# Kernel optimization log

Measured on AMD Instinct MI355X. Metric: run time of the kernel, lower is better.

The kernel has to match this reference:

```python
import jax, jax.numpy as jnp
import numpy as np

B, K, E = 32768, 100, 64
N_USERS, N_ITEMS = 100000, 50000
MLP_DIMS = [2, 20, 200, 200, 20, 1]  # input_dim=2 -> x10 -> x100 -> x100 -> x10 -> output_dim=1


def setup_inputs() -> dict:
    key = jax.random.key(0)
    ks = jax.random.split(key, 20)
    inp = {
        "user_idxs": jax.random.randint(ks[0], (B,), 0, N_USERS),
        "item_idxs": jax.random.randint(ks[1], (B,), 0, N_ITEMS),
        "user_idx_tensor": jax.random.randint(ks[2], (N_USERS, K), 0, N_USERS),
        "item_idx_tensor": jax.random.randint(ks[3], (N_ITEMS, K), 0, N_ITEMS),
        # nn.Embedding default init: N(0, 1)
        "user_emb": jax.random.normal(ks[4], (N_USERS, E), dtype=jnp.float32),
        "item_emb": jax.random.normal(ks[5], (N_ITEMS, E), dtype=jnp.float32),
    }
    # nn.Linear default init: U(-1/sqrt(fan_in), 1/sqrt(fan_in))
    for i in range(5):
        fan_in, fan_out = MLP_DIMS[i], MLP_DIMS[i + 1]
        bound = 1.0 / np.sqrt(fan_in)
        inp[f"w{i+1}"] = jax.random.uniform(ks[6 + i], (fan_out, fan_in), minval=-bound, maxval=bound, dtype=jnp.float32)
        inp[f"b{i+1}"] = jax.random.uniform(ks[11 + i], (fan_out,), minval=-bound, maxval=bound, dtype=jnp.float32)
    return inp


def _concat_mlp(x, w1, b1, w2, b2, w3, b3, w4, b4, w5, b5):
    # x: [B, E, 2] -> [B, E, 1]
    h = jax.nn.relu(x @ w1.T + b1)
    h = jax.nn.relu(h @ w2.T + b2)
    h = jax.nn.relu(h @ w3.T + b3)
    h = jax.nn.relu(h @ w4.T + b4)
    return h @ w5.T + b5


def reference(user_idxs, item_idxs, user_idx_tensor, item_idx_tensor,
              user_emb, item_emb,
              w1, b1, w2, b2, w3, b3, w4, b4, w5, b5):
    user_neighs = user_idx_tensor[user_idxs]          # [B, K]
    user_sum = user_emb[user_neighs].sum(axis=1)      # [B, E]
    item_neighs = item_idx_tensor[item_idxs]          # [B, K]
    item_sum = item_emb[item_neighs].sum(axis=1)      # [B, E]
    # cat along dim 1 with keepdim then permute(0,2,1) == stack along last axis
    x = jnp.stack([user_sum, item_sum], axis=-1)      # [B, E, 2]
    concat = _concat_mlp(x, w1, b1, w2, b2, w3, b3, w4, b4, w5, b5)  # [B, E, 1]
    return jax.nn.sigmoid(concat.mean(axis=1)).squeeze(-1)           # [B]
```

## Files before the change

kernel.cpp:

```cpp
#include <hip/hip_runtime.h>
#include <hip/hip_bf16.h>
#include <math.h>

typedef short v8s __attribute__((ext_vector_type(8)));
typedef float v4f __attribute__((ext_vector_type(4)));
typedef unsigned int v4u __attribute__((ext_vector_type(4)));
typedef unsigned short us;
typedef unsigned int uu;

#define MFMA16(a,b,c) __builtin_amdgcn_mfma_f32_16x16x32_bf16((a),(b),(c),0,0,0)

#define W3F_ELEMS (7*13*512)
#define W2F_ELEMS (13*512)
#define W4F_ELEMS (14*512)
#define WALL_ELEMS (W3F_ELEMS + W2F_ELEMS + W4F_ELEMS)
#define OFF_W3F 0
#define OFF_W2F (OFF_W3F + W3F_ELEMS*2)
#define OFF_W4F (OFF_W2F + W2F_ELEMS*2)
#define OFF_B2B (OFF_W4F + W4F_ELEMS*2)
#define OFF_B3B (OFF_B2B + 208*4)
#define OFF_B4B (OFF_B3B + 224*4)
#define OFF_W5B (OFF_B4B + 32*4)
#define OFF_W1P (OFF_W5B + 32*4)
#define OFF_X   (256*1024)
#define CB_ELEMS 592
#define CB_B3 208
#define CB_B4 432
#define CB_W5 464
#define CB_W1 496

__device__ __forceinline__ us f2bf(float f) {
    union { float f; unsigned int u; } v; v.f = f;
    unsigned int u = v.u + 0x7FFFu + ((v.u >> 16) & 1u);
    return (us)(u >> 16);
}
__device__ __forceinline__ uu pack2bf(float a, float b) {
    union { __hip_bfloat162 v; uu u; } cv;
    cv.v.x = __float2bfloat16(a);
    cv.v.y = __float2bfloat16(b);
    return cv.u;
}
__device__ __forceinline__ us f2h(float f) {
    _Float16 h = (_Float16)f;
    return *(us*)&h;
}

__global__ void prep_conv_kernel(
    const float* __restrict__ w1, const float* __restrict__ b1,
    const float* __restrict__ w2, const float* __restrict__ w3,
    const float* __restrict__ w4, const float* __restrict__ b2,
    const float* __restrict__ b3, const float* __restrict__ b4,
    const float* __restrict__ w5, char* __restrict__ ws,
    const float* __restrict__ uemb, const float* __restrict__ iemb,
    _Float16* __restrict__ ue16, _Float16* __restrict__ ie16,
    int nu64, int ni64)
{
    us* w3f = (us*)(ws + OFF_W3F);
    us* w2f = (us*)(ws + OFF_W2F);
    us* w4f = (us*)(ws + OFF_W4F);
    float* b2b = (float*)(ws + OFF_B2B);
    float* b3b = (float*)(ws + OFF_B3B);
    float* b4b = (float*)(ws + OFF_B4B);
    float* w5b = (float*)(ws + OFF_W5B);
    float* w1p = (float*)(ws + OFF_W1P);

    const int gid = blockIdx.x * blockDim.x + threadIdx.x;
    const int stride = gridDim.x * blockDim.x;

    for (int i = gid*4; i < nu64; i += stride*4) {
        float4 v = *(const float4*)(uemb + i);
        ushort4 o = { f2h(v.x), f2h(v.y), f2h(v.z), f2h(v.w) };
        *(ushort4*)((us*)ue16 + i) = o;
    }
    for (int i = gid*4; i < ni64; i += stride*4) {
        float4 v = *(const float4*)(iemb + i);
        ushort4 o = { f2h(v.x), f2h(v.y), f2h(v.z), f2h(v.w) };
        *(ushort4*)((us*)ie16 + i) = o;
    }

    for (int idx = gid; idx < W3F_ELEMS; idx += stride) {
        int i = idx & 7, lane = (idx >> 3) & 63, f = idx >> 9;
        int nt3 = f % 13, t = f / 13;
        int cc = lane & 15, gg = lane >> 4;
        int j = 16*nt3 + cc;
        int k = 32*t + 16*(i >> 2) + 4*gg + (i & 3);
        w3f[idx] = f2bf((j < 200 && k < 200) ? w3[j*200 + k] : 0.f);
    }
    for (int idx = gid; idx < W2F_ELEMS; idx += stride) {
        int i = idx & 7, lane = (idx >> 3) & 63, nt = idx >> 9;
        int j = 16*nt + (lane & 15), k = 8*(lane >> 4) + i;
        w2f[idx] = f2bf((j < 200 && k < 20) ? w2[j*20 + k] : 0.f);
    }
    for (int idx = gid; idx < W4F_ELEMS; idx += stride) {
        int i = idx & 7, lane = (idx >> 3) & 63, f = idx >> 9;
        int t = f >> 1, jt = f & 1;
        int cc = lane & 15, gg = lane >> 4;
        int j = 16*jt + cc;
        int k = 32*t + 16*(i >> 2) + 4*gg + (i & 3);
        w4f[idx] = f2bf((j < 20 && k < 200) ? w4[j*200 + k] : 0.f);
    }
    for (int i = gid; i < 208; i += stride) b2b[i] = (i < 200) ? b2[i] : 0.f;
    for (int i = gid; i < 224; i += stride) b3b[i] = (i < 200) ? b3[i] : 0.f;
    for (int i = gid; i < 32;  i += stride) b4b[i] = (i < 20) ? b4[i] : 0.f;
    for (int i = gid; i < 32;  i += stride) w5b[i] = (i < 20) ? w5[i] : 0.f;
    for (int i = gid; i < 96;  i += stride) {
        int q = i >> 5, r = i & 31;
        float v = 0.f;
        if (r < 20) v = (q == 0) ? w1[2*r] : (q == 1) ? w1[2*r + 1] : b1[r];
        w1p[i] = v;
    }
}

__global__ __launch_bounds__(256, 8) void gather_kernel(
    const int* __restrict__ user_idxs, const int* __restrict__ item_idxs,
    const int* __restrict__ uidx, const int* __restrict__ iidx,
    const _Float16* __restrict__ ue16, const _Float16* __restrict__ ie16,
    float* __restrict__ xu, float* __restrict__ xi, int B)
{
    const int tid  = (int)threadIdx.x;
    const int lane = tid & 63;
    const int task = (int)blockIdx.x * 4 + (tid >> 6);
    if (task >= 2*B) return;
    const int b = task >> 1;
    const bool isItem = task & 1;

    const int* nrow = isItem ? (iidx + (size_t)item_idxs[b]*100)
                             : (uidx + (size_t)user_idxs[b]*100);
    const _Float16* emb = isItem ? ie16 : ue16;

    float a0=0.f,a1=0.f,a2=0.f,a3=0.f,a4=0.f,a5=0.f,a6=0.f,a7=0.f;
    #pragma unroll 2
    for (int k = 0; k < 96; k += 16) {
        int4 i0 = *(const int4*)(nrow + k);
        int4 i1 = *(const int4*)(nrow + k + 4);
        int4 i2 = *(const int4*)(nrow + k + 8);
        int4 i3 = *(const int4*)(nrow + k + 12);
        a0 += (float)emb[(size_t)i0.x*64 + lane];
        a1 += (float)emb[(size_t)i0.y*64 + lane];
        a2 += (float)emb[(size_t)i0.z*64 + lane];
        a3 += (float)emb[(size_t)i0.w*64 + lane];
        a4 += (float)emb[(size_t)i1.x*64 + lane];
        a5 += (float)emb[(size_t)i1.y*64 + lane];
        a6 += (float)emb[(size_t)i1.z*64 + lane];
        a7 += (float)emb[(size_t)i1.w*64 + lane];
        a0 += (float)emb[(size_t)i2.x*64 + lane];
        a1 += (float)emb[(size_t)i2.y*64 + lane];
        a2 += (float)emb[(size_t)i2.z*64 + lane];
        a3 += (float)emb[(size_t)i2.w*64 + lane];
        a4 += (float)emb[(size_t)i3.x*64 + lane];
        a5 += (float)emb[(size_t)i3.y*64 + lane];
        a6 += (float)emb[(size_t)i3.z*64 + lane];
        a7 += (float)emb[(size_t)i3.w*64 + lane];
    }
    int4 it = *(const int4*)(nrow + 96);
    a0 += (float)emb[(size_t)it.x*64 + lane];
    a1 += (float)emb[(size_t)it.y*64 + lane];
    a2 += (float)emb[(size_t)it.z*64 + lane];
    a3 += (float)emb[(size_t)it.w*64 + lane];

    float s = ((a0+a4)+(a1+a5)) + ((a2+a6)+(a3+a7));
    (isItem ? xi : xu)[(size_t)b*64 + lane] = s;
}

__device__ __forceinline__ void make_b1f4(float su, float si, int c, int g,
                                          const float* __restrict__ w1p,
                                          v4u b1f[4])
{
    const v4f wx0 = *(const v4f*)(w1p + 8*g);
    const v4f wx1 = *(const v4f*)(w1p + 8*g + 4);
    const v4f wy0 = *(const v4f*)(w1p + 32 + 8*g);
    const v4f wy1 = *(const v4f*)(w1p + 32 + 8*g + 4);
    const v4f wb0 = *(const v4f*)(w1p + 64 + 8*g);
    const v4f wb1 = *(const v4f*)(w1p + 64 + 8*g + 4);
    #pragma unroll
    for (int m = 0; m < 4; ++m) {
        const float xu = __shfl(su, 16*m + c);
        const float xv = __shfl(si, 16*m + c);
        float h0 = fmaxf(fmaf(xu, wx0[0], fmaf(xv, wy0[0], wb0[0])), 0.f);
        float h1 = fmaxf(fmaf(xu, wx0[1], fmaf(xv, wy0[1], wb0[1])), 0.f);
        float h2 = fmaxf(fmaf(xu, wx0[2], fmaf(xv, wy0[2], wb0[2])), 0.f);
        float h3 = fmaxf(fmaf(xu, wx0[3], fmaf(xv, wy0[3], wb0[3])), 0.f);
        float h4 = fmaxf(fmaf(xu, wx1[0], fmaf(xv, wy1[0], wb1[0])), 0.f);
        float h5 = fmaxf(fmaf(xu, wx1[1], fmaf(xv, wy1[1], wb1[1])), 0.f);
        float h6 = fmaxf(fmaf(xu, wx1[2], fmaf(xv, wy1[2], wb1[2])), 0.f);
        float h7 = fmaxf(fmaf(xu, wx1[3], fmaf(xv, wy1[3], wb1[3])), 0.f);
        b1f[m] = (v4u){ pack2bf(h0,h1), pack2bf(h2,h3),
                        pack2bf(h4,h5), pack2bf(h6,h7) };
    }
}

__global__ __launch_bounds__(512, 2) void mlp_kernel(
    const float* __restrict__ xu, const float* __restrict__ xi,
    const float* __restrict__ b5p, const char* __restrict__ ws,
    float* __restrict__ out, int B, int NIT)
{
    __shared__ us wall[WALL_ELEMS];
    __shared__ __align__(16) float cbuf[CB_ELEMS];

    const int tid  = (int)threadIdx.x;
    const int lane = tid & 63;
    const int wv   = __builtin_amdgcn_readfirstlane(tid >> 6);
    const int c = lane & 15;
    const int g = lane >> 4;
    const int wstep = (int)gridDim.x * 8;

    {
        const us* src = (const us*)(ws + OFF_W3F);
        for (int s = tid; s < WALL_ELEMS/8; s += 512)
            *(v8s*)(wall + s*8) = *(const v8s*)(src + s*8);
        const float* csrc = (const float*)(ws + OFF_B2B);
        for (int s = tid; s < CB_ELEMS; s += 512)
            cbuf[s] = csrc[s];
    }
    const us* w3l = wall;
    const us* w2l = wall + W3F_ELEMS;
    const us* w4l = wall + W3F_ELEMS + W2F_ELEMS;
    const float b5v = b5p[0];

    int b = (int)blockIdx.x*8 + wv;
    int bc = (b < B) ? b : (B - 1);
    float su = xu[(size_t)bc*64 + lane];
    float si = xi[(size_t)bc*64 + lane];
    __syncthreads();

    #pragma unroll 1
    for (int it = 0; it < NIT; ++it) {
        const int nb = b + wstep;
        const int nbc = (nb < B) ? nb : (B - 1);
        const bool more = (it + 1 < NIT);

        v4u b1f[4];
        make_b1f4(su, si, c, g, cbuf + CB_W1, b1f);

        v4u b2f[4][7];
        __builtin_amdgcn_s_setprio(1);
        #pragma unroll
        for (int t = 0; t < 6; ++t) {
            v8s afa = *(const v8s*)(w2l + ((2*t)*64   + lane)*8);
            v8s afb = *(const v8s*)(w2l + ((2*t+1)*64 + lane)*8);
            v4f bva = *(const v4f*)(cbuf + 32*t + 4*g);
            v4f bvb = *(const v4f*)(cbuf + 32*t + 16 + 4*g);
            #pragma unroll
            for (int m = 0; m < 4; ++m) {
                v8s bb = __builtin_bit_cast(v8s, b1f[m]);
                v4f aa = MFMA16(afa, bb, bva);
                v4f ab = MFMA16(afb, bb, bvb);
                b2f[m][t] = (v4u){ pack2bf(fmaxf(aa[0],0.f), fmaxf(aa[1],0.f)),
                                   pack2bf(fmaxf(aa[2],0.f), fmaxf(aa[3],0.f)),
                                   pack2bf(fmaxf(ab[0],0.f), fmaxf(ab[1],0.f)),
                                   pack2bf(fmaxf(ab[2],0.f), fmaxf(ab[3],0.f)) };
            }
        }
        {
            v8s afa = *(const v8s*)(w2l + (12*64 + lane)*8);
            v4f bva = *(const v4f*)(cbuf + 192 + 4*g);
            #pragma unroll
            for (int m = 0; m < 4; ++m) {
                v8s bb = __builtin_bit_cast(v8s, b1f[m]);
                v4f aa = MFMA16(afa, bb, bva);
                b2f[m][6] = (v4u){ pack2bf(fmaxf(aa[0],0.f), fmaxf(aa[1],0.f)),
                                   pack2bf(fmaxf(aa[2],0.f), fmaxf(aa[3],0.f)),
                                   0u, 0u };
            }
        }
        __builtin_amdgcn_s_setprio(0);

        float nsu = 0.f, nsi = 0.f;
        if (more) {
            nsu = xu[(size_t)nbc*64 + lane];
            nsi = xi[(size_t)nbc*64 + lane];
        }

        v4f acc4[4][2];
        v4f bc0 = *(const v4f*)(cbuf + CB_B4 + 4*g);
        v4f bc1 = *(const v4f*)(cbuf + CB_B4 + 16 + 4*g);
        #pragma unroll
        for (int p = 0; p < 7; ++p) {
            v8s a40 = *(const v8s*)(w4l + ((2*p)*64   + lane)*8);
            v8s a41 = *(const v8s*)(w4l + ((2*p+1)*64 + lane)*8);

            v4f acc3[4][2];
            __builtin_amdgcn_s_setprio(1);
            {
                v8s af0 = *(const v8s*)(w3l + ((2*p)*64 + lane)*8);
                v4f bv0 = *(const v4f*)(cbuf + CB_B3 + 16*(2*p) + 4*g);
                #pragma unroll
                for (int m = 0; m < 4; ++m)
                    acc3[m][0] = MFMA16(af0, __builtin_bit_cast(v8s, b2f[m][0]), bv0);
                if (p < 6) {
                    v8s af1 = *(const v8s*)(w3l + ((2*p+1)*64 + lane)*8);
                    v4f bv1 = *(const v4f*)(cbuf + CB_B3 + 16*(2*p+1) + 4*g);
                    #pragma unroll
                    for (int m = 0; m < 4; ++m)
                        acc3[m][1] = MFMA16(af1, __builtin_bit_cast(v8s, b2f[m][0]), bv1);
                }
            }
            #pragma unroll
            for (int ksc = 1; ksc < 7; ++ksc) {
                v8s af0 = *(const v8s*)(w3l + ((ksc*13 + 2*p)*64 + lane)*8);
                #pragma unroll
                for (int m = 0; m < 4; ++m)
                    acc3[m][0] = MFMA16(af0, __builtin_bit_cast(v8s, b2f[m][ksc]), acc3[m][0]);
                if (p < 6) {
                    v8s af1 = *(const v8s*)(w3l + ((ksc*13 + 2*p+1)*64 + lane)*8);
                    #pragma unroll
                    for (int m = 0; m < 4; ++m)
                        acc3[m][1] = MFMA16(af1, __builtin_bit_cast(v8s, b2f[m][ksc]), acc3[m][1]);
                }
            }
            __builtin_amdgcn_s_setprio(0);
            #pragma unroll
            for (int m = 0; m < 4; ++m) {
                v4u bfu;
                if (p < 6) {
                    bfu = (v4u){
                        pack2bf(fmaxf(acc3[m][0][0],0.f), fmaxf(acc3[m][0][1],0.f)),
                        pack2bf(fmaxf(acc3[m][0][2],0.f), fmaxf(acc3[m][0][3],0.f)),
                        pack2bf(fmaxf(acc3[m][1][0],0.f), fmaxf(acc3[m][1][1],0.f)),
                        pack2bf(fmaxf(acc3[m][1][2],0.f), fmaxf(acc3[m][1][3],0.f)) };
                } else {
                    bfu = (v4u){
                        pack2bf(fmaxf(acc3[m][0][0],0.f), fmaxf(acc3[m][0][1],0.f)),
                        pack2bf(fmaxf(acc3[m][0][2],0.f), fmaxf(acc3[m][0][3],0.f)),
                        0u, 0u };
                }
                v8s bb = __builtin_bit_cast(v8s, bfu);
                acc4[m][0] = MFMA16(a40, bb, (p == 0) ? bc0 : acc4[m][0]);
                acc4[m][1] = MFMA16(a41, bb, (p == 0) ? bc1 : acc4[m][1]);
            }
        }

        __builtin_amdgcn_sched_barrier(0);

        v4f w5lo = *(const v4f*)(cbuf + CB_W5 + 4*g);
        v4f w5hi = *(const v4f*)(cbuf + CB_W5 + 16 + 4*g);
        float s = 0.f;
        #pragma unroll
        for (int m = 0; m < 4; ++m) {
            #pragma unroll
            for (int q = 0; q < 4; ++q) {
                float h0 = fmaxf(acc4[m][0][q], 0.f);
                float h1 = fmaxf(acc4[m][1][q], 0.f);
                s = fmaf(h0, w5lo[q], fmaf(h1, w5hi[q], s));
            }
        }
        #pragma unroll
        for (int off = 1; off < 64; off <<= 1) s += __shfl_xor(s, off);
        if (lane == 0 && b < B)
            out[b] = 1.0f / (1.0f + expf(-(s * (1.0f / 64.0f) + b5v)));

        su = nsu; si = nsi; b = nb;
    }
}

extern "C" void kernel_launch(void* const* d_in, const int* in_sizes, int n_in,
                              void* d_out, int out_size, void* d_ws, size_t ws_size,
                              hipStream_t stream) {
    const int*   user_idxs = (const int*)d_in[0];
    const int*   item_idxs = (const int*)d_in[1];
    const int*   uidx      = (const int*)d_in[2];
    const int*   iidx      = (const int*)d_in[3];
    const float* uemb      = (const float*)d_in[4];
    const float* iemb      = (const float*)d_in[5];
    const float* w1 = (const float*)d_in[6];
    const float* b1 = (const float*)d_in[7];
    const float* w2 = (const float*)d_in[8];
    const float* b2 = (const float*)d_in[9];
    const float* w3 = (const float*)d_in[10];
    const float* b3 = (const float*)d_in[11];
    const float* w4 = (const float*)d_in[12];
    const float* b4 = (const float*)d_in[13];
    const float* w5 = (const float*)d_in[14];
    const float* b5 = (const float*)d_in[15];
    float* out = (float*)d_out;
    char* ws = (char*)d_ws;

    const int B    = in_sizes[0];
    const int nu64 = in_sizes[4];
    const int ni64 = in_sizes[5];

    float* xu = (float*)(ws + OFF_X);
    float* xi = xu + (size_t)B * 64;
    _Float16* ue16 = (_Float16*)(ws + OFF_X + (size_t)2 * B * 64 * 4);
    _Float16* ie16 = ue16 + nu64;

    hipLaunchKernelGGL(prep_conv_kernel, dim3(1024), dim3(256), 0, stream,
                       w1, b1, w2, w3, w4, b2, b3, b4, w5, ws,
                       uemb, iemb, ue16, ie16, nu64, ni64);

    const int ntask = 2 * B;
    hipLaunchKernelGGL(gather_kernel, dim3((ntask + 3) / 4), dim3(256), 0, stream,
                       user_idxs, item_idxs, uidx, iidx, ue16, ie16, xu, xi, B);

    const int GRID = 256;
    const int rows_per_iter = GRID * 8;
    const int NIT = (B + rows_per_iter - 1) / rows_per_iter;
    hipLaunchKernelGGL(mlp_kernel, dim3(GRID), dim3(512), 0, stream,
                       xu, xi, b5, ws, out, B, NIT);
}
```

Baseline: 326.6 us.

## Split per-row MLP into two half passes to cut registers and raise waves per block

The MLP body now handles each batch row's 64 embedding dims in two passes of 32 instead of one pass of 64, which halves the live b2f/acc3/acc4 register arrays. This register saving is used to raise the block size from 512 to 768 threads (12 waves, 12 rows per block per iteration) with launch bounds (768,3). The aim is more resident waves to hide MFMA and LDS latency. In exchange each pass reloads the weight fragments from LDS twice per row, and the next-row prefetch is now issued between the two passes.

```diff
diff --git a/kernel.cpp b/kernel.cpp
--- a/kernel.cpp
+++ b/kernel.cpp
@@ -162,9 +162,10 @@
     (isItem ? xi : xu)[(size_t)b*64 + lane] = s;
 }
 
-__device__ __forceinline__ void make_b1f4(float su, float si, int c, int g,
+template <int P>
+__device__ __forceinline__ void make_b1f2(float su, float si, int c, int g,
                                           const float* __restrict__ w1p,
-                                          v4u b1f[4])
+                                          v4u b1f[2])
 {
     const v4f wx0 = *(const v4f*)(w1p + 8*g);
     const v4f wx1 = *(const v4f*)(w1p + 8*g + 4);
@@ -173,9 +174,9 @@
     const v4f wb0 = *(const v4f*)(w1p + 64 + 8*g);
     const v4f wb1 = *(const v4f*)(w1p + 64 + 8*g + 4);
     #pragma unroll
-    for (int m = 0; m < 4; ++m) {
-        const float xu = __shfl(su, 16*m + c);
-        const float xv = __shfl(si, 16*m + c);
+    for (int m = 0; m < 2; ++m) {
+        const float xu = __shfl(su, 32*P + 16*m + c);
+        const float xv = __shfl(si, 32*P + 16*m + c);
         float h0 = fmaxf(fmaf(xu, wx0[0], fmaf(xv, wy0[0], wb0[0])), 0.f);
         float h1 = fmaxf(fmaf(xu, wx0[1], fmaf(xv, wy0[1], wb0[1])), 0.f);
         float h2 = fmaxf(fmaf(xu, wx0[2], fmaf(xv, wy0[2], wb0[2])), 0.f);
@@ -189,7 +190,119 @@
     }
 }
 
-__global__ __launch_bounds__(512, 2) void mlp_kernel(
+__device__ __forceinline__ float mlp_pass2(
+    const v4u b1f[2],
+    const us* __restrict__ w3l, const us* __restrict__ w2l,
+    const us* __restrict__ w4l, const float* __restrict__ cbuf,
+    const int lane, const int g)
+{
+    const v8s bb0 = __builtin_bit_cast(v8s, b1f[0]);
+    const v8s bb1 = __builtin_bit_cast(v8s, b1f[1]);
+
+    v4u b2f[2][7];
+    __builtin_amdgcn_s_setprio(1);
+    #pragma unroll
+    for (int t = 0; t < 6; ++t) {
+        v8s afa = *(const v8s*)(w2l + ((2*t)*64   + lane)*8);
+        v8s afb = *(const v8s*)(w2l + ((2*t+1)*64 + lane)*8);
+        v4f bva = *(const v4f*)(cbuf + 32*t + 4*g);
+        v4f bvb = *(const v4f*)(cbuf + 32*t + 16 + 4*g);
+        v4f aa0 = MFMA16(afa, bb0, bva);
+        v4f aa1 = MFMA16(afa, bb1, bva);
+        v4f ab0 = MFMA16(afb, bb0, bvb);
+        v4f ab1 = MFMA16(afb, bb1, bvb);
+        b2f[0][t] = (v4u){ pack2bf(fmaxf(aa0[0],0.f), fmaxf(aa0[1],0.f)),
+                           pack2bf(fmaxf(aa0[2],0.f), fmaxf(aa0[3],0.f)),
+                           pack2bf(fmaxf(ab0[0],0.f), fmaxf(ab0[1],0.f)),
+                           pack2bf(fmaxf(ab0[2],0.f), fmaxf(ab0[3],0.f)) };
+        b2f[1][t] = (v4u){ pack2bf(fmaxf(aa1[0],0.f), fmaxf(aa1[1],0.f)),
+                           pack2bf(fmaxf(aa1[2],0.f), fmaxf(aa1[3],0.f)),
+                           pack2bf(fmaxf(ab1[0],0.f), fmaxf(ab1[1],0.f)),
+                           pack2bf(fmaxf(ab1[2],0.f), fmaxf(ab1[3],0.f)) };
+    }
+    {
+        v8s afa = *(const v8s*)(w2l + (12*64 + lane)*8);
+        v4f bva = *(const v4f*)(cbuf + 192 + 4*g);
+        v4f aa0 = MFMA16(afa, bb0, bva);
+        v4f aa1 = MFMA16(afa, bb1, bva);
+        b2f[0][6] = (v4u){ pack2bf(fmaxf(aa0[0],0.f), fmaxf(aa0[1],0.f)),
+                           pack2bf(fmaxf(aa0[2],0.f), fmaxf(aa0[3],0.f)), 0u, 0u };
+        b2f[1][6] = (v4u){ pack2bf(fmaxf(aa1[0],0.f), fmaxf(aa1[1],0.f)),
+                           pack2bf(fmaxf(aa1[2],0.f), fmaxf(aa1[3],0.f)), 0u, 0u };
+    }
+    __builtin_amdgcn_s_setprio(0);
+
+    v4f acc4[2][2];
+    v4f bc0 = *(const v4f*)(cbuf + CB_B4 + 4*g);
+    v4f bc1 = *(const v4f*)(cbuf + CB_B4 + 16 + 4*g);
+    #pragma unroll
+    for (int p = 0; p < 7; ++p) {
+        v8s a40 = *(const v8s*)(w4l + ((2*p)*64   + lane)*8);
+        v8s a41 = *(const v8s*)(w4l + ((2*p+1)*64 + lane)*8);
+
+        v4f acc3[2][2];
+        __builtin_amdgcn_s_setprio(1);
+        {
+            v8s af0 = *(const v8s*)(w3l + ((2*p)*64 + lane)*8);
+            v4f bv0 = *(const v4f*)(cbuf + CB_B3 + 16*(2*p) + 4*g);
+            acc3[0][0] = MFMA16(af0, __builtin_bit_cast(v8s, b2f[0][0]), bv0);
+            acc3[1][0] = MFMA16(af0, __builtin_bit_cast(v8s, b2f[1][0]), bv0);
+            if (p < 6) {
+                v8s af1 = *(const v8s*)(w3l + ((2*p+1)*64 + lane)*8);
+                v4f bv1 = *(const v4f*)(cbuf + CB_B3 + 16*(2*p+1) + 4*g);
+                acc3[0][1] = MFMA16(af1, __builtin_bit_cast(v8s, b2f[0][0]), bv1);
+                acc3[1][1] = MFMA16(af1, __builtin_bit_cast(v8s, b2f[1][0]), bv1);
+            }
+        }
+        #pragma unroll
+        for (int ksc = 1; ksc < 7; ++ksc) {
+            v8s af0 = *(const v8s*)(w3l + ((ksc*13 + 2*p)*64 + lane)*8);
+            acc3[0][0] = MFMA16(af0, __builtin_bit_cast(v8s, b2f[0][ksc]), acc3[0][0]);
+            acc3[1][0] = MFMA16(af0, __builtin_bit_cast(v8s, b2f[1][ksc]), acc3[1][0]);
+            if (p < 6) {
+                v8s af1 = *(const v8s*)(w3l + ((ksc*13 + 2*p+1)*64 + lane)*8);
+                acc3[0][1] = MFMA16(af1, __builtin_bit_cast(v8s, b2f[0][ksc]), acc3[0][1]);
+                acc3[1][1] = MFMA16(af1, __builtin_bit_cast(v8s, b2f[1][ksc]), acc3[1][1]);
+            }
+        }
+        __builtin_amdgcn_s_setprio(0);
+        #pragma unroll
+        for (int m = 0; m < 2; ++m) {
+            v4u bfu;
+            if (p < 6) {
+                bfu = (v4u){
+                    pack2bf(fmaxf(acc3[m][0][0],0.f), fmaxf(acc3[m][0][1],0.f)),
+                    pack2bf(fmaxf(acc3[m][0][2],0.f), fmaxf(acc3[m][0][3],0.f)),
+                    pack2bf(fmaxf(acc3[m][1][0],0.f), fmaxf(acc3[m][1][1],0.f)),
+                    pack2bf(fmaxf(acc3[m][1][2],0.f), fmaxf(acc3[m][1][3],0.f)) };
+            } else {
+                bfu = (v4u){
+                    pack2bf(fmaxf(acc3[m][0][0],0.f), fmaxf(acc3[m][0][1],0.f)),
+                    pack2bf(fmaxf(acc3[m][0][2],0.f), fmaxf(acc3[m][0][3],0.f)),
+                    0u, 0u };
+            }
+            v8s bb = __builtin_bit_cast(v8s, bfu);
+            acc4[m][0] = MFMA16(a40, bb, (p == 0) ? bc0 : acc4[m][0]);
+            acc4[m][1] = MFMA16(a41, bb, (p == 0) ? bc1 : acc4[m][1]);
+        }
+    }
+
+    v4f w5lo = *(const v4f*)(cbuf + CB_W5 + 4*g);
+    v4f w5hi = *(const v4f*)(cbuf + CB_W5 + 16 + 4*g);
+    float s = 0.f;
+    #pragma unroll
+    for (int m = 0; m < 2; ++m) {
+        #pragma unroll
+        for (int q = 0; q < 4; ++q) {
+            float h0 = fmaxf(acc4[m][0][q], 0.f);
+            float h1 = fmaxf(acc4[m][1][q], 0.f);
+            s = fmaf(h0, w5lo[q], fmaf(h1, w5hi[q], s));
+        }
+    }
+    return s;
+}
+
+__global__ __launch_bounds__(768, 3) void mlp_kernel(
     const float* __restrict__ xu, const float* __restrict__ xi,
     const float* __restrict__ b5p, const char* __restrict__ ws,
     float* __restrict__ out, int B, int NIT)
@@ -202,14 +315,14 @@
     const int wv   = __builtin_amdgcn_readfirstlane(tid >> 6);
     const int c = lane & 15;
     const int g = lane >> 4;
-    const int wstep = (int)gridDim.x * 8;
+    const int wstep = (int)gridDim.x * 12;
 
     {
         const us* src = (const us*)(ws + OFF_W3F);
-        for (int s = tid; s < WALL_ELEMS/8; s += 512)
+        for (int s = tid; s < WALL_ELEMS/8; s += 768)
             *(v8s*)(wall + s*8) = *(const v8s*)(src + s*8);
         const float* csrc = (const float*)(ws + OFF_B2B);
-        for (int s = tid; s < CB_ELEMS; s += 512)
+        for (int s = tid; s < CB_ELEMS; s += 768)
             cbuf[s] = csrc[s];
     }
     const us* w3l = wall;
@@ -217,7 +330,7 @@
     const us* w4l = wall + W3F_ELEMS + W2F_ELEMS;
     const float b5v = b5p[0];
 
-    int b = (int)blockIdx.x*8 + wv;
+    int b = (int)blockIdx.x*12 + wv;
     int bc = (b < B) ? b : (B - 1);
     float su = xu[(size_t)bc*64 + lane];
     float si = xi[(size_t)bc*64 + lane];
@@ -229,121 +342,22 @@
         const int nbc = (nb < B) ? nb : (B - 1);
         const bool more = (it + 1 < NIT);
 
-        v4u b1f[4];
-        make_b1f4(su, si, c, g, cbuf + CB_W1, b1f);
-
-        v4u b2f[4][7];
-        __builtin_amdgcn_s_setprio(1);
-        #pragma unroll
-        for (int t = 0; t < 6; ++t) {
-            v8s afa = *(const v8s*)(w2l + ((2*t)*64   + lane)*8);
-            v8s afb = *(const v8s*)(w2l + ((2*t+1)*64 + lane)*8);
-            v4f bva = *(const v4f*)(cbuf + 32*t + 4*g);
-            v4f bvb = *(const v4f*)(cbuf + 32*t + 16 + 4*g);
-            #pragma unroll
-            for (int m = 0; m < 4; ++m) {
-                v8s bb = __builtin_bit_cast(v8s, b1f[m]);
-                v4f aa = MFMA16(afa, bb, bva);
-                v4f ab = MFMA16(afb, bb, bvb);
-                b2f[m][t] = (v4u){ pack2bf(fmaxf(aa[0],0.f), fmaxf(aa[1],0.f)),
-                                   pack2bf(fmaxf(aa[2],0.f), fmaxf(aa[3],0.f)),
-                                   pack2bf(fmaxf(ab[0],0.f), fmaxf(ab[1],0.f)),
-                                   pack2bf(fmaxf(ab[2],0.f), fmaxf(ab[3],0.f)) };
-            }
-        }
-        {
-            v8s afa = *(const v8s*)(w2l + (12*64 + lane)*8);
-            v4f bva = *(const v4f*)(cbuf + 192 + 4*g);
-            #pragma unroll
-            for (int m = 0; m < 4; ++m) {
-                v8s bb = __builtin_bit_cast(v8s, b1f[m]);
-                v4f aa = MFMA16(afa, bb, bva);
-                b2f[m][6] = (v4u){ pack2bf(fmaxf(aa[0],0.f), fmaxf(aa[1],0.f)),
-                                   pack2bf(fmaxf(aa[2],0.f), fmaxf(aa[3],0.f)),
-                                   0u, 0u };
-            }
-        }
-        __builtin_amdgcn_s_setprio(0);
+        v4u b1f[2];
+        make_b1f2<0>(su, si, c, g, cbuf + CB_W1, b1f);
+        float s = mlp_pass2(b1f, w3l, w2l, w4l, cbuf, lane, g);
+
+        __builtin_amdgcn_sched_barrier(0);
 
         float nsu = 0.f, nsi = 0.f;
         if (more) {
             nsu = xu[(size_t)nbc*64 + lane];
             nsi = xi[(size_t)nbc*64 + lane];
         }
-
-        v4f acc4[4][2];
-        v4f bc0 = *(const v4f*)(cbuf + CB_B4 + 4*g);
-        v4f bc1 = *(const v4f*)(cbuf + CB_B4 + 16 + 4*g);
-        #pragma unroll
-        for (int p = 0; p < 7; ++p) {
-            v8s a40 = *(const v8s*)(w4l + ((2*p)*64   + lane)*8);
-            v8s a41 = *(const v8s*)(w4l + ((2*p+1)*64 + lane)*8);
-
-            v4f acc3[4][2];
-            __builtin_amdgcn_s_setprio(1);
-            {
-                v8s af0 = *(const v8s*)(w3l + ((2*p)*64 + lane)*8);
-                v4f bv0 = *(const v4f*)(cbuf + CB_B3 + 16*(2*p) + 4*g);
-                #pragma unroll
-                for (int m = 0; m < 4; ++m)
-                    acc3[m][0] = MFMA16(af0, __builtin_bit_cast(v8s, b2f[m][0]), bv0);
-                if (p < 6) {
-                    v8s af1 = *(const v8s*)(w3l + ((2*p+1)*64 + lane)*8);
-                    v4f bv1 = *(const v4f*)(cbuf + CB_B3 + 16*(2*p+1) + 4*g);
-                    #pragma unroll
-                    for (int m = 0; m < 4; ++m)
-                        acc3[m][1] = MFMA16(af1, __builtin_bit_cast(v8s, b2f[m][0]), bv1);
-                }
-            }
-            #pragma unroll
-            for (int ksc = 1; ksc < 7; ++ksc) {
-                v8s af0 = *(const v8s*)(w3l + ((ksc*13 + 2*p)*64 + lane)*8);
-                #pragma unroll
-                for (int m = 0; m < 4; ++m)
-                    acc3[m][0] = MFMA16(af0, __builtin_bit_cast(v8s, b2f[m][ksc]), acc3[m][0]);
-                if (p < 6) {
-                    v8s af1 = *(const v8s*)(w3l + ((ksc*13 + 2*p+1)*64 + lane)*8);
-                    #pragma unroll
-                    for (int m = 0; m < 4; ++m)
-                        acc3[m][1] = MFMA16(af1, __builtin_bit_cast(v8s, b2f[m][ksc]), acc3[m][1]);
-                }
-            }
-            __builtin_amdgcn_s_setprio(0);
-            #pragma unroll
-            for (int m = 0; m < 4; ++m) {
-                v4u bfu;
-                if (p < 6) {
-                    bfu = (v4u){
-                        pack2bf(fmaxf(acc3[m][0][0],0.f), fmaxf(acc3[m][0][1],0.f)),
-                        pack2bf(fmaxf(acc3[m][0][2],0.f), fmaxf(acc3[m][0][3],0.f)),
-                        pack2bf(fmaxf(acc3[m][1][0],0.f), fmaxf(acc3[m][1][1],0.f)),
-                        pack2bf(fmaxf(acc3[m][1][2],0.f), fmaxf(acc3[m][1][3],0.f)) };
-                } else {
-                    bfu = (v4u){
-                        pack2bf(fmaxf(acc3[m][0][0],0.f), fmaxf(acc3[m][0][1],0.f)),
-                        pack2bf(fmaxf(acc3[m][0][2],0.f), fmaxf(acc3[m][0][3],0.f)),
-                        0u, 0u };
-                }
-                v8s bb = __builtin_bit_cast(v8s, bfu);
-                acc4[m][0] = MFMA16(a40, bb, (p == 0) ? bc0 : acc4[m][0]);
-                acc4[m][1] = MFMA16(a41, bb, (p == 0) ? bc1 : acc4[m][1]);
-            }
-        }
+        make_b1f2<1>(su, si, c, g, cbuf + CB_W1, b1f);
+        s += mlp_pass2(b1f, w3l, w2l, w4l, cbuf, lane, g);
 
         __builtin_amdgcn_sched_barrier(0);
 
-        v4f w5lo = *(const v4f*)(cbuf + CB_W5 + 4*g);
-        v4f w5hi = *(const v4f*)(cbuf + CB_W5 + 16 + 4*g);
-        float s = 0.f;
-        #pragma unroll
-        for (int m = 0; m < 4; ++m) {
-            #pragma unroll
-            for (int q = 0; q < 4; ++q) {
-                float h0 = fmaxf(acc4[m][0][q], 0.f);
-                float h1 = fmaxf(acc4[m][1][q], 0.f);
-                s = fmaf(h0, w5lo[q], fmaf(h1, w5hi[q], s));
-            }
-        }
         #pragma unroll
         for (int off = 1; off < 64; off <<= 1) s += __shfl_xor(s, off);
         if (lane == 0 && b < B)
@@ -393,8 +407,8 @@
                        user_idxs, item_idxs, uidx, iidx, ue16, ie16, xu, xi, B);
 
     const int GRID = 256;
-    const int rows_per_iter = GRID * 8;
+    const int rows_per_iter = GRID * 12;
     const int NIT = (B + rows_per_iter - 1) / rows_per_iter;
-    hipLaunchKernelGGL(mlp_kernel, dim3(GRID), dim3(512), 0, stream,
+    hipLaunchKernelGGL(mlp_kernel, dim3(GRID), dim3(768), 0, stream,
                        xu, xi, b5, ws, out, B, NIT);
 }
```

Result: slower. 337.1 us (+3.2%).
